# Kernel optimization log

Hardware: AMD Instinct MI355X
Metric: run time of the kernel (lower is better)

Reference implementation:

```python
import jax, jax.numpy as jnp
import numpy as np

N, D, L = 200000, 256, 4  # nodes, feature dim, num_levels


def _l2norm(x, eps=1e-12):
    # matches F.normalize(p=2, dim=-1): x / max(||x||, eps)
    n = jnp.linalg.norm(x, axis=-1, keepdims=True)
    return x / jnp.clip(n, eps)


def setup_inputs() -> dict:
    key = jax.random.key(0)
    ks = jax.random.split(key, 6)
    inp = {}
    for i in range(4):
        inp[f"x{i}"] = jax.random.normal(ks[i], (N, D), dtype=jnp.float32)
    # nn.Linear(2*dim, 1): weight [1, 2D] stored here as vector [2D], bias [1]
    bound = 1.0 / float(np.sqrt(2 * D))
    inp["w_att"] = jax.random.uniform(ks[4], (2 * D,), jnp.float32, -bound, bound)
    inp["b_att"] = jax.random.uniform(ks[5], (1,), jnp.float32, -bound, bound)
    return inp


def reference(x0, x1, x2, x3, w_att, b_att):
    # ATT branch, eval mode (dropout is identity at inference)
    d = x0.shape[-1]
    query_n = _l2norm(x0)                       # [N, D]
    msgs = _l2norm(jnp.stack([x1, x2, x3]))     # [L-1, N, D], normalized messages
    # lin_att(cat((message, query), -1)) == message @ w_m + query @ w_q + b
    w_m, w_q = w_att[:d], w_att[d:]
    score = (jnp.einsum('lnd,d->ln', msgs, w_m)
             + query_n @ w_q + b_att[0])        # [L-1, N]
    score = jax.nn.leaky_relu(score, negative_slope=0.01)
    # segment softmax over index[1] = range(N)*(L-1): exactly softmax over level axis
    score = jax.nn.softmax(score, axis=0)       # [L-1, N]
    # scatter-add of score * message per node == weighted sum over levels
    embedding = x0 + jnp.einsum('ln,lnd->nd', score, msgs)  # [N, D]
    # flatten score to match cat-order of message rows ([x1 rows; x2 rows; x3 rows])
    return embedding, score.reshape(-1)
```

## Files before the change

kernel.cpp:

```cpp
#include <hip/hip_runtime.h>

#define D 256
#define F4_PER_ROW (D / 4)

__device__ __forceinline__ float dot4(float4 a, float4 b) {
    return fmaf(a.x, b.x, fmaf(a.y, b.y, fmaf(a.z, b.z, a.w * b.w)));
}

__global__ __launch_bounds__(256) void merge_xs_kernel(
    const float* __restrict__ x0, const float* __restrict__ x1,
    const float* __restrict__ x2, const float* __restrict__ x3,
    const float* __restrict__ w_att, const float* __restrict__ b_att,
    float* __restrict__ emb, float* __restrict__ sc_out, int N)
{
    const int lane = threadIdx.x & 63;
    const int wid  = threadIdx.x >> 6;
    const int wpb  = blockDim.x >> 6;
    const int rstride = gridDim.x * wpb;

    const float4 wm = reinterpret_cast<const float4*>(w_att)[lane];
    const float4 wq = reinterpret_cast<const float4*>(w_att)[64 + lane];
    const float b = b_att[0];

    for (int row = blockIdx.x * wpb + wid; row < N; row += rstride) {
        const size_t base = (size_t)row * F4_PER_ROW + lane;
        float4 v0 = reinterpret_cast<const float4*>(x0)[base];
        float4 v1 = reinterpret_cast<const float4*>(x1)[base];
        float4 v2 = reinterpret_cast<const float4*>(x2)[base];
        float4 v3 = reinterpret_cast<const float4*>(x3)[base];

        float r0 = dot4(v0, v0);
        float r1 = dot4(v0, wq);
        float r2 = dot4(v1, v1);
        float r3 = dot4(v1, wm);
        float r4 = dot4(v2, v2);
        float r5 = dot4(v2, wm);
        float r6 = dot4(v3, v3);
        float r7 = dot4(v3, wm);

        #pragma unroll
        for (int off = 32; off > 0; off >>= 1) {
            r0 += __shfl_xor(r0, off, 64);
            r1 += __shfl_xor(r1, off, 64);
            r2 += __shfl_xor(r2, off, 64);
            r3 += __shfl_xor(r3, off, 64);
            r4 += __shfl_xor(r4, off, 64);
            r5 += __shfl_xor(r5, off, 64);
            r6 += __shfl_xor(r6, off, 64);
            r7 += __shfl_xor(r7, off, 64);
        }

        const float n0 = fmaxf(sqrtf(r0), 1e-12f);
        const float n1 = fmaxf(sqrtf(r2), 1e-12f);
        const float n2 = fmaxf(sqrtf(r4), 1e-12f);
        const float n3 = fmaxf(sqrtf(r6), 1e-12f);

        const float qterm = r1 / n0 + b;
        float s1 = r3 / n1 + qterm;
        float s2 = r5 / n2 + qterm;
        float s3 = r7 / n3 + qterm;

        s1 = s1 > 0.f ? s1 : 0.01f * s1;
        s2 = s2 > 0.f ? s2 : 0.01f * s2;
        s3 = s3 > 0.f ? s3 : 0.01f * s3;

        const float m  = fmaxf(s1, fmaxf(s2, s3));
        const float e1 = expf(s1 - m);
        const float e2 = expf(s2 - m);
        const float e3 = expf(s3 - m);
        const float inv = 1.0f / (e1 + e2 + e3);
        const float sc1 = e1 * inv, sc2 = e2 * inv, sc3 = e3 * inv;

        const float c1 = sc1 / n1, c2 = sc2 / n2, c3 = sc3 / n3;
        float4 o;
        o.x = fmaf(c1, v1.x, fmaf(c2, v2.x, fmaf(c3, v3.x, v0.x)));
        o.y = fmaf(c1, v1.y, fmaf(c2, v2.y, fmaf(c3, v3.y, v0.y)));
        o.z = fmaf(c1, v1.z, fmaf(c2, v2.z, fmaf(c3, v3.z, v0.z)));
        o.w = fmaf(c1, v1.w, fmaf(c2, v2.w, fmaf(c3, v3.w, v0.w)));
        reinterpret_cast<float4*>(emb)[base] = o;

        if (lane == 0) {
            sc_out[row]         = sc1;
            sc_out[N + row]     = sc2;
            sc_out[2 * N + row] = sc3;
        }
    }
}

extern "C" void kernel_launch(void* const* d_in, const int* in_sizes, int n_in,
                              void* d_out, int out_size, void* d_ws, size_t ws_size,
                              hipStream_t stream) {
    const float* x0    = (const float*)d_in[0];
    const float* x1    = (const float*)d_in[1];
    const float* x2    = (const float*)d_in[2];
    const float* x3    = (const float*)d_in[3];
    const float* w_att = (const float*)d_in[4];
    const float* b_att = (const float*)d_in[5];

    const int N = in_sizes[0] / D;
    float* emb = (float*)d_out;
    float* sc  = emb + (size_t)N * D;

    const int threads = 256;
    const int wpb = threads / 64;
    int blocks = (N + wpb - 1) / wpb;
    if (blocks > 4096) blocks = 4096;

    merge_xs_kernel<<<blocks, threads, 0, stream>>>(x0, x1, x2, x3, w_att, b_att,
                                                    emb, sc, N);
}
```

Measured before the change: 220.6 us.

## Process two rows per wave with half-wave split and nontemporal stores

Each wave now handles two rows, one per 32-lane half. Each lane loads two float4s per input and the shuffle reduction runs over 16 lanes instead of 32. The output embedding and score writes use nontemporal stores so the write-once streams do not pollute the cache. This raises memory-level parallelism per lane and cuts reduction overhead, at the cost of more registers per thread.

```diff
diff --git a/kernel.cpp b/kernel.cpp
--- a/kernel.cpp
+++ b/kernel.cpp
@@ -3,8 +3,15 @@
 #define D 256
 #define F4_PER_ROW (D / 4)
 
+typedef float fx4 __attribute__((ext_vector_type(4)));
+
 __device__ __forceinline__ float dot4(float4 a, float4 b) {
     return fmaf(a.x, b.x, fmaf(a.y, b.y, fmaf(a.z, b.z, a.w * b.w)));
+}
+
+__device__ __forceinline__ void nt_store4(float4 v, float4* p) {
+    fx4 t; t.x = v.x; t.y = v.y; t.z = v.z; t.w = v.w;
+    __builtin_nontemporal_store(t, reinterpret_cast<fx4*>(p));
 }
 
 __global__ __launch_bounds__(256) void merge_xs_kernel(
@@ -14,32 +21,48 @@
     float* __restrict__ emb, float* __restrict__ sc_out, int N)
 {
     const int lane = threadIdx.x & 63;
+    const int sub  = lane & 31;
+    const int half = lane >> 5;
     const int wid  = threadIdx.x >> 6;
     const int wpb  = blockDim.x >> 6;
-    const int rstride = gridDim.x * wpb;
+    const int nwaves = gridDim.x * wpb;
+    const int gw   = blockIdx.x * wpb + wid;
 
-    const float4 wm = reinterpret_cast<const float4*>(w_att)[lane];
-    const float4 wq = reinterpret_cast<const float4*>(w_att)[64 + lane];
+    const float4* x0f = reinterpret_cast<const float4*>(x0);
+    const float4* x1f = reinterpret_cast<const float4*>(x1);
+    const float4* x2f = reinterpret_cast<const float4*>(x2);
+    const float4* x3f = reinterpret_cast<const float4*>(x3);
+    float4* embf      = reinterpret_cast<float4*>(emb);
+
+    const float4* wmf = reinterpret_cast<const float4*>(w_att);
+    const float4* wqf = wmf + 32 * 2;
+    const float4 wma = wmf[sub], wmb = wmf[sub + 32];
+    const float4 wqa = wqf[sub], wqb = wqf[sub + 32];
     const float b = b_att[0];
 
-    for (int row = blockIdx.x * wpb + wid; row < N; row += rstride) {
-        const size_t base = (size_t)row * F4_PER_ROW + lane;
-        float4 v0 = reinterpret_cast<const float4*>(x0)[base];
-        float4 v1 = reinterpret_cast<const float4*>(x1)[base];
-        float4 v2 = reinterpret_cast<const float4*>(x2)[base];
-        float4 v3 = reinterpret_cast<const float4*>(x3)[base];
+    const int nUnits = (N + 1) >> 1;
 
-        float r0 = dot4(v0, v0);
-        float r1 = dot4(v0, wq);
-        float r2 = dot4(v1, v1);
-        float r3 = dot4(v1, wm);
-        float r4 = dot4(v2, v2);
-        float r5 = dot4(v2, wm);
-        float r6 = dot4(v3, v3);
-        float r7 = dot4(v3, wm);
+    for (int unit = gw; unit < nUnits; unit += nwaves) {
+        const int row = unit * 2 + half;
+        const bool valid = row < N;
+        const size_t base = valid ? ((size_t)row * F4_PER_ROW + sub) : (size_t)sub;
+
+        float4 v0a = x0f[base], v0b = x0f[base + 32];
+        float4 v1a = x1f[base], v1b = x1f[base + 32];
+        float4 v2a = x2f[base], v2b = x2f[base + 32];
+        float4 v3a = x3f[base], v3b = x3f[base + 32];
+
+        float r0 = dot4(v0a, v0a) + dot4(v0b, v0b);
+        float r1 = dot4(v0a, wqa) + dot4(v0b, wqb);
+        float r2 = dot4(v1a, v1a) + dot4(v1b, v1b);
+        float r3 = dot4(v1a, wma) + dot4(v1b, wmb);
+        float r4 = dot4(v2a, v2a) + dot4(v2b, v2b);
+        float r5 = dot4(v2a, wma) + dot4(v2b, wmb);
+        float r6 = dot4(v3a, v3a) + dot4(v3b, v3b);
+        float r7 = dot4(v3a, wma) + dot4(v3b, wmb);
 
         #pragma unroll
-        for (int off = 32; off > 0; off >>= 1) {
+        for (int off = 16; off > 0; off >>= 1) {
             r0 += __shfl_xor(r0, off, 64);
             r1 += __shfl_xor(r1, off, 64);
             r2 += __shfl_xor(r2, off, 64);
@@ -72,17 +95,24 @@
         const float sc1 = e1 * inv, sc2 = e2 * inv, sc3 = e3 * inv;
 
         const float c1 = sc1 / n1, c2 = sc2 / n2, c3 = sc3 / n3;
-        float4 o;
-        o.x = fmaf(c1, v1.x, fmaf(c2, v2.x, fmaf(c3, v3.x, v0.x)));
-        o.y = fmaf(c1, v1.y, fmaf(c2, v2.y, fmaf(c3, v3.y, v0.y)));
-        o.z = fmaf(c1, v1.z, fmaf(c2, v2.z, fmaf(c3, v3.z, v0.z)));
-        o.w = fmaf(c1, v1.w, fmaf(c2, v2.w, fmaf(c3, v3.w, v0.w)));
-        reinterpret_cast<float4*>(emb)[base] = o;
+        float4 oa, ob;
+        oa.x = fmaf(c1, v1a.x, fmaf(c2, v2a.x, fmaf(c3, v3a.x, v0a.x)));
+        oa.y = fmaf(c1, v1a.y, fmaf(c2, v2a.y, fmaf(c3, v3a.y, v0a.y)));
+        oa.z = fmaf(c1, v1a.z, fmaf(c2, v2a.z, fmaf(c3, v3a.z, v0a.z)));
+        oa.w = fmaf(c1, v1a.w, fmaf(c2, v2a.w, fmaf(c3, v3a.w, v0a.w)));
+        ob.x = fmaf(c1, v1b.x, fmaf(c2, v2b.x, fmaf(c3, v3b.x, v0b.x)));
+        ob.y = fmaf(c1, v1b.y, fmaf(c2, v2b.y, fmaf(c3, v3b.y, v0b.y)));
+        ob.z = fmaf(c1, v1b.z, fmaf(c2, v2b.z, fmaf(c3, v3b.z, v0b.z)));
+        ob.w = fmaf(c1, v1b.w, fmaf(c2, v2b.w, fmaf(c3, v3b.w, v0b.w)));
 
-        if (lane == 0) {
-            sc_out[row]         = sc1;
-            sc_out[N + row]     = sc2;
-            sc_out[2 * N + row] = sc3;
+        if (valid) {
+            nt_store4(oa, &embf[base]);
+            nt_store4(ob, &embf[base + 32]);
+            if (sub == 0) {
+                __builtin_nontemporal_store(sc1, &sc_out[row]);
+                __builtin_nontemporal_store(sc2, &sc_out[N + row]);
+                __builtin_nontemporal_store(sc3, &sc_out[2 * N + row]);
+            }
         }
     }
 }
@@ -103,7 +133,8 @@
 
     const int threads = 256;
     const int wpb = threads / 64;
-    int blocks = (N + wpb - 1) / wpb;
+    const int nUnits = (N + 1) / 2;
+    int blocks = (nUnits + wpb - 1) / wpb;
     if (blocks > 4096) blocks = 4096;
 
     merge_xs_kernel<<<blocks, threads, 0, stream>>>(x0, x1, x2, x3, w_att, b_att,
```

New measurement: 206.3 us. 6.5% less time.
